# Optimization experiments

Hardware: AMD Instinct MI355X
Metric: run time of the kernel (lower is better)

Reference implementation:

```python
import jax, jax.numpy as jnp
import numpy as np

B, S, E, H = 2, 2048, 1024, 16
D = E // H
LN_EPS = 1e-5
NORM_EPS = 1e-12  # F.normalize clamp_min


def setup_inputs() -> dict:
    key = jax.random.key(0)
    ks = jax.random.split(key, 4)
    x = jax.random.normal(ks[0], (B, S, E), dtype=jnp.float32)
    qkv_w = jax.random.normal(ks[1], (3 * E, E), dtype=jnp.float32) * 0.02
    qkv_b = jnp.zeros((3 * E,), dtype=jnp.float32)
    out_w = jax.random.normal(ks[2], (E, E), dtype=jnp.float32) * 0.02
    out_b = jnp.zeros((E,), dtype=jnp.float32)
    ln_w = jnp.ones((E,), dtype=jnp.float32)
    ln_b = jnp.zeros((E,), dtype=jnp.float32)
    qknorm_scale = jnp.asarray(E ** -0.5, dtype=jnp.float32)
    # RotaryEmbedding buffer: inv_freq interleaved (emb[::2] = emb[1::2] = base**(-arange(0,E,2)/E))
    base_freq = 10000.0 ** (-(np.arange(0, E, 2).astype(np.float32) / E))
    emb = np.empty((E,), dtype=np.float32)
    emb[::2] = base_freq
    emb[1::2] = base_freq
    inv_freq = jnp.asarray(emb)
    return {"x": x, "ln_w": ln_w, "ln_b": ln_b, "qkv_w": qkv_w, "qkv_b": qkv_b,
            "qknorm_scale": qknorm_scale, "out_w": out_w, "out_b": out_b, "inv_freq": inv_freq}


def _rotate(t, sin, cos):
    # Faithful to source: x1 = even idx (excluding last), x2 = odd idx; cat(-x2, x1)
    x1 = t[..., :-1:2]
    x2 = t[..., 1::2]
    t_rot = jnp.concatenate((-x2, x1), axis=-1)
    return t * cos + t_rot * sin


def _l2norm(t):
    n = jnp.sqrt(jnp.sum(t * t, axis=-1, keepdims=True))
    return t / jnp.maximum(n, NORM_EPS)


def reference(x, ln_w, ln_b, qkv_w, qkv_b, qknorm_scale, out_w, out_b, inv_freq):
    # --- prenorm (LayerNorm, eps=1e-5) ---
    mu = jnp.mean(x, axis=-1, keepdims=True)
    var = jnp.mean((x - mu) ** 2, axis=-1, keepdims=True)
    xn = (x - mu) / jnp.sqrt(var + LN_EPS) * ln_w + ln_b
    # --- QKV projection ---
    qkv = xn @ qkv_w.T + qkv_b  # [B,S,3E]
    q, k, v = jnp.split(qkv, 3, axis=-1)
    # --- rotary (source uses scalar seq*inv_freq, not per-position) ---
    seq = q.shape[1]
    sin = jnp.sin(seq * inv_freq)
    cos = jnp.cos(seq * inv_freq)
    q = _rotate(q, sin, cos)
    k = _rotate(k, sin, cos)
    # --- split heads: [B,S,E] -> [B,H,S,D] ---
    split = lambda t: t.reshape(B, seq, H, D).transpose(0, 2, 1, 3)
    q, k, v = split(q), split(k), split(v)
    # --- qknorm ---
    q = _l2norm(q) * qknorm_scale
    k = _l2norm(k) * qknorm_scale
    # --- scaled dot product with causal mask ---
    aw = jnp.einsum('bhqd,bhkd->bhqk', q, k)  # [B,H,S,S]
    causal = jnp.tril(jnp.ones((seq, seq), dtype=bool))
    aw = jnp.where(causal, aw, jnp.finfo(aw.dtype).min)
    aw = jax.nn.softmax(aw, axis=-1)
    attn = jnp.einsum('bhqk,bhkd->bhqd', aw, v)
    # --- merge heads + out proj ---
    attn = attn.transpose(0, 2, 1, 3).reshape(B, seq, E)
    return attn @ out_w.T + out_b
```

## Files before the change

kernel.cpp:

```cpp
#include <hip/hip_runtime.h>

typedef unsigned short u16;
typedef __attribute__((ext_vector_type(8))) short bf16x8;
typedef __attribute__((ext_vector_type(4))) float f32x4;

#define SS 2048
#define EE 1024
#define HH 16
#define DD 64

__device__ __forceinline__ float b2f(u16 u) {
  union { unsigned int i; float f; } v; v.i = ((unsigned int)u) << 16; return v.f;
}
__device__ __forceinline__ u16 f2b(float f) {
  union { float f; unsigned int i; } v; v.f = f;
  unsigned int i = v.i;
  return (u16)((i + 0x7FFFu + ((i >> 16) & 1u)) >> 16);
}
__device__ __forceinline__ unsigned int cvt_pk_bf16(float lo, float hi) {
  unsigned int r;
  asm("v_cvt_pk_bf16_f32 %0, %1, %2" : "=v"(r) : "v"(lo), "v"(hi));
  return r;
}

#define GLD16(g, l)                                                         \
  __builtin_amdgcn_global_load_lds(                                         \
      (const __attribute__((address_space(1))) unsigned int*)(g),           \
      (__attribute__((address_space(3))) unsigned int*)(l), 16, 0, 0)

__global__ __launch_bounds__(256) void k_prep(const float* __restrict__ qkv_w,
                                              u16* __restrict__ wq_b,
                                              const float* __restrict__ inv_freq,
                                              float2* __restrict__ cs,
                                              const float* __restrict__ x,
                                              const float* __restrict__ lw,
                                              const float* __restrict__ lb,
                                              u16* __restrict__ xn) {
  const int bx = blockIdx.x, t = threadIdx.x;
  if (bx < 3072) {
    const int i = bx * 256 + t;
    float4 v = ((const float4*)qkv_w)[i];
    ushort4 o;
    o.x = f2b(v.x); o.y = f2b(v.y); o.z = f2b(v.z); o.w = f2b(v.w);
    ((ushort4*)wq_b)[i] = o;
    return;
  }
  if (bx < 3076) {
    const int i = (bx - 3072) * 256 + t;
    float th = 2048.0f * inv_freq[i];
    cs[i] = make_float2(cosf(th), sinf(th));
    return;
  }
  const int row = bx - 3076;
  float4 v = ((const float4*)(x + (size_t)row * EE))[t];
  float f0 = v.x, f1 = v.y, f2 = v.z, f3 = v.w;
  float s = f0 + f1 + f2 + f3;
  float ss = f0 * f0 + f1 * f1 + f2 * f2 + f3 * f3;
  for (int o = 1; o < 64; o <<= 1) { s += __shfl_xor(s, o); ss += __shfl_xor(ss, o); }
  __shared__ float red[8];
  int w = t >> 6;
  if ((t & 63) == 0) { red[w] = s; red[4 + w] = ss; }
  __syncthreads();
  s = red[0] + red[1] + red[2] + red[3];
  ss = red[4] + red[5] + red[6] + red[7];
  float mu = s * (1.0f / 1024.0f);
  float var = ss * (1.0f / 1024.0f) - mu * mu;
  float rstd = rsqrtf(var + 1e-5f);
  float4 wv = ((const float4*)lw)[t];
  float4 bv = ((const float4*)lb)[t];
  ushort4 o;
  o.x = f2b((f0 - mu) * rstd * wv.x + bv.x);
  o.y = f2b((f1 - mu) * rstd * wv.y + bv.y);
  o.z = f2b((f2 - mu) * rstd * wv.z + bv.z);
  o.w = f2b((f3 - mu) * rstd * wv.w + bv.w);
  ((ushort4*)(xn + (size_t)row * EE))[t] = o;
}

__global__ __launch_bounds__(256) void k_gemm_b(const u16* __restrict__ A,
                                                const u16* __restrict__ W,
                                                const float* __restrict__ bias,
                                                u16* __restrict__ C,
                                                int M, int N, int K) {
  __shared__ __align__(16) u16 As[128 * 32];
  __shared__ __align__(16) u16 Ws[128 * 32];
  const int t = threadIdx.x;
  const int m0 = blockIdx.y * 128, n0 = blockIdx.x * 128;
  const int lane = t & 63, w = t >> 6, quad = lane >> 4, l15 = lane & 15;
  const int wm = (w & 1) * 64, wn = (w >> 1) * 64;

  f32x4 zero4 = {0.f, 0.f, 0.f, 0.f};
  f32x4 acc[4][4];
  for (int mi = 0; mi < 4; mi++)
    for (int ni = 0; ni < 4; ni++) acc[mi][ni] = zero4;

  const u16* Ag = A + (size_t)(m0 + (t >> 2)) * K + (t & 3) * 8;
  const u16* Wg = W + (size_t)(n0 + (t >> 2)) * K + (t & 3) * 8;
  const size_t rowskip = (size_t)64 * K;

  for (int k0 = 0; k0 < K; k0 += 32) {
    GLD16(Ag + k0, As + t * 8);
    GLD16(Ag + rowskip + k0, As + 2048 + t * 8);
    GLD16(Wg + k0, Ws + t * 8);
    GLD16(Wg + rowskip + k0, Ws + 2048 + t * 8);
    __syncthreads();
    bf16x8 af[4], wf[4];
#pragma unroll
    for (int i = 0; i < 4; i++) {
      af[i] = *(const bf16x8*)(As + (wm + i * 16 + l15) * 32 + quad * 8);
      wf[i] = *(const bf16x8*)(Ws + (wn + i * 16 + l15) * 32 + quad * 8);
    }
#pragma unroll
    for (int mi = 0; mi < 4; mi++)
#pragma unroll
      for (int ni = 0; ni < 4; ni++)
        acc[mi][ni] = __builtin_amdgcn_mfma_f32_16x16x32_bf16(af[mi], wf[ni], acc[mi][ni], 0, 0, 0);
    __syncthreads();
  }
  for (int mi = 0; mi < 4; mi++)
    for (int ni = 0; ni < 4; ni++) {
      int col = n0 + wn + ni * 16 + l15;
      float bb = bias[col];
      for (int r = 0; r < 4; r++) {
        int grow = m0 + wm + mi * 16 + quad * 4 + r;
        C[(size_t)grow * N + col] = f2b(acc[mi][ni][r] + bb);
      }
    }
}

__global__ __launch_bounds__(256) void k_gemm_fw(const u16* __restrict__ A,
                                                 const float* __restrict__ W,
                                                 const float* __restrict__ bias,
                                                 float* __restrict__ C,
                                                 int M, int N, int K) {
  __shared__ __align__(16) u16 As[64 * 32];
  __shared__ __align__(16) u16 Ws[128 * 32];
  const int t = threadIdx.x;
  const int m0 = blockIdx.y * 64, n0 = blockIdx.x * 128;
  const int lane = t & 63, w = t >> 6, quad = lane >> 4, l15 = lane & 15;
  const int wm = (w & 1) * 32, wn = (w >> 1) * 64;

  f32x4 zero4 = {0.f, 0.f, 0.f, 0.f};
  f32x4 acc[2][4];
  for (int mi = 0; mi < 2; mi++)
    for (int ni = 0; ni < 4; ni++) acc[mi][ni] = zero4;

  const u16* Ag = A + (size_t)(m0 + (t >> 2)) * K + (t & 3) * 8;
  const float* Wg0 = W + (size_t)(n0 + (t >> 2)) * K + (t & 3) * 8;
  const float* Wg1 = Wg0 + (size_t)64 * K;

  for (int k0 = 0; k0 < K; k0 += 32) {
    GLD16(Ag + k0, As + t * 8);
    float4 wa = *(const float4*)(Wg0 + k0);
    float4 wb = *(const float4*)(Wg0 + k0 + 4);
    float4 wc = *(const float4*)(Wg1 + k0);
    float4 wd = *(const float4*)(Wg1 + k0 + 4);
    union { unsigned int u[4]; bf16x8 v8; } p0, p1;
    p0.u[0] = cvt_pk_bf16(wa.x, wa.y); p0.u[1] = cvt_pk_bf16(wa.z, wa.w);
    p0.u[2] = cvt_pk_bf16(wb.x, wb.y); p0.u[3] = cvt_pk_bf16(wb.z, wb.w);
    p1.u[0] = cvt_pk_bf16(wc.x, wc.y); p1.u[1] = cvt_pk_bf16(wc.z, wc.w);
    p1.u[2] = cvt_pk_bf16(wd.x, wd.y); p1.u[3] = cvt_pk_bf16(wd.z, wd.w);
    *(bf16x8*)(Ws + t * 8) = p0.v8;
    *(bf16x8*)(Ws + 2048 + t * 8) = p1.v8;
    __syncthreads();
    bf16x8 af[2], wf[4];
#pragma unroll
    for (int i = 0; i < 2; i++)
      af[i] = *(const bf16x8*)(As + (wm + i * 16 + l15) * 32 + quad * 8);
#pragma unroll
    for (int i = 0; i < 4; i++)
      wf[i] = *(const bf16x8*)(Ws + (wn + i * 16 + l15) * 32 + quad * 8);
#pragma unroll
    for (int mi = 0; mi < 2; mi++)
#pragma unroll
      for (int ni = 0; ni < 4; ni++)
        acc[mi][ni] = __builtin_amdgcn_mfma_f32_16x16x32_bf16(af[mi], wf[ni], acc[mi][ni], 0, 0, 0);
    __syncthreads();
  }
  for (int mi = 0; mi < 2; mi++)
    for (int ni = 0; ni < 4; ni++) {
      int col = n0 + wn + ni * 16 + l15;
      float bb = bias[col];
      for (int r = 0; r < 4; r++) {
        int grow = m0 + wm + mi * 16 + quad * 4 + r;
        C[(size_t)grow * N + col] = acc[mi][ni][r] + bb;
      }
    }
}

__global__ __launch_bounds__(256) void k_rotv(u16* __restrict__ qkv,
                                              const float2* __restrict__ cs_tab,
                                              const float* __restrict__ scale_p,
                                              u16* __restrict__ vt) {
  __shared__ float qf[1024];
  __shared__ float kf[1024];
  __shared__ __align__(16) u16 tile[64 * 72];
  const int row = blockIdx.x, t = threadIdx.x;
  {
    u16* qr = qkv + (size_t)row * 3072;
    u16* kr = qr + 1024;
    ushort4 qv = ((const ushort4*)qr)[t];
    ushort4 kv = ((const ushort4*)kr)[t];
    *(float4*)(qf + 4 * t) = make_float4(b2f(qv.x), b2f(qv.y), b2f(qv.z), b2f(qv.w));
    *(float4*)(kf + 4 * t) = make_float4(b2f(kv.x), b2f(kv.y), b2f(kv.z), b2f(kv.w));
    __syncthreads();
    const float scale = scale_p[0];
    float rq[4], rk[4];
#pragma unroll
    for (int u = 0; u < 4; u++) {
      int j = 4 * t + u;
      float2 cs = cs_tab[j];
      float qrot = (j < 512) ? -qf[2 * j + 1] : qf[2 * (j - 512)];
      float krot = (j < 512) ? -kf[2 * j + 1] : kf[2 * (j - 512)];
      rq[u] = qf[j] * cs.x + qrot * cs.y;
      rk[u] = kf[j] * cs.x + krot * cs.y;
    }
    float ssq = rq[0] * rq[0] + rq[1] * rq[1] + rq[2] * rq[2] + rq[3] * rq[3];
    float ssk = rk[0] * rk[0] + rk[1] * rk[1] + rk[2] * rk[2] + rk[3] * rk[3];
    for (int o = 1; o < 16; o <<= 1) { ssq += __shfl_xor(ssq, o); ssk += __shfl_xor(ssk, o); }
    float qs = scale / fmaxf(sqrtf(ssq), 1e-12f);
    float ks = scale / fmaxf(sqrtf(ssk), 1e-12f);
    ushort4 qo, ko;
    qo.x = f2b(rq[0] * qs); qo.y = f2b(rq[1] * qs); qo.z = f2b(rq[2] * qs); qo.w = f2b(rq[3] * qs);
    ko.x = f2b(rk[0] * ks); ko.y = f2b(rk[1] * ks); ko.z = f2b(rk[2] * ks); ko.w = f2b(rk[3] * ks);
    ((ushort4*)qr)[t] = qo;
    ((ushort4*)kr)[t] = ko;
  }
  if (row >= 1024) return;
  const int st = row & 31, bh = row >> 5;
  const int b = bh >> 4, h = bh & 15;
  const int s0 = st * 64;
  const int si = t >> 2, dc = t & 3;
  __syncthreads();
  const u16* src = qkv + (size_t)(b * SS + s0 + si) * 3072 + 2048 + h * DD;
  bf16x8 v0 = *(const bf16x8*)(src + dc * 8);
  bf16x8 v1 = *(const bf16x8*)(src + (dc + 4) * 8);
#pragma unroll
  for (int u = 0; u < 8; u++) tile[(dc * 8 + u) * 72 + si] = (u16)v0[u];
#pragma unroll
  for (int u = 0; u < 8; u++) tile[((dc + 4) * 8 + u) * 72 + si] = (u16)v1[u];
  __syncthreads();
#pragma unroll
  for (int it = 0; it < 2; it++) {
    int idx = t + it * 256;
    int d = idx >> 3, ch = idx & 7;
    bf16x8 o = *(const bf16x8*)(tile + d * 72 + ch * 8);
    *(bf16x8*)(vt + (size_t)(bh * DD + d) * SS + s0 + ch * 8) = o;
  }
}

__global__ __launch_bounds__(512, 4) void k_attn(const u16* __restrict__ qkv,
                                                 const u16* __restrict__ vt,
                                                 u16* __restrict__ out) {
  __shared__ __align__(16) u16 Kt[2][128 * 72];
  __shared__ __align__(16) u16 Vt[2][64 * 136];
  const int bh = blockIdx.x;
  const int y = blockIdx.y;
  const int qt = (y < 8) ? y : 23 - y;
  const int b = bh >> 4, h = bh & 15;
  const int t = threadIdx.x, w = t >> 6, lane = t & 63, quad = lane >> 4, l15 = lane & 15;
  const int krow = t >> 2, kq = (t & 3) * 16;
  const int dr = t >> 3, kc8 = t & 7;
  const int srcl = (lane & 48) + ((lane >> 4) << 2);
  const int qA = ((lane >> 4) & 1) * 32 + l15;
  const int qB = qA + 16;
  const bool hiN = (quad >> 1) & 1;
  const u16* kn = qkv + 1024;
  f32x4 zero4 = {0.f, 0.f, 0.f, 0.f};
  const int q0 = qt * 128;

  bf16x8 qf[2];
  {
    const u16* qrow = qkv + (size_t)(b * SS + q0 + 16 * w + l15) * 3072 + h * DD;
    qf[0] = *(const bf16x8*)(qrow + quad * 8);
    qf[1] = *(const bf16x8*)(qrow + 32 + quad * 8);
  }
  f32x4 oacc[4];
  for (int n = 0; n < 4; n++) oacc[n] = zero4;
  float m_i = -1e30f, l_i = 0.f;

  bf16x8 kv[2], vv[2];
  {
    const u16* krg = kn + (size_t)(b * SS + krow) * 3072 + h * DD + kq;
    kv[0] = *(const bf16x8*)(krg);
    kv[1] = *(const bf16x8*)(krg + 8);
    const u16* vrg = vt + (size_t)(bh * DD + dr) * SS + kc8 * 16;
    vv[0] = *(const bf16x8*)(vrg);
    vv[1] = *(const bf16x8*)(vrg + 8);
  }
  *(bf16x8*)(Kt[0] + krow * 72 + kq) = kv[0];
  *(bf16x8*)(Kt[0] + krow * 72 + kq + 8) = kv[1];
  *(bf16x8*)(Vt[0] + dr * 136 + kc8 * 16) = vv[0];
  *(bf16x8*)(Vt[0] + dr * 136 + kc8 * 16 + 8) = vv[1];
  __syncthreads();
  int cur = 0;

  for (int kt = 0; kt <= qt; kt++) {
    if (kt < qt) {
      const int k0n = (kt + 1) * 128;
      const u16* krg = kn + (size_t)(b * SS + k0n + krow) * 3072 + h * DD + kq;
      kv[0] = *(const bf16x8*)(krg);
      kv[1] = *(const bf16x8*)(krg + 8);
      const u16* vrg = vt + (size_t)(bh * DD + dr) * SS + k0n + kc8 * 16;
      vv[0] = *(const bf16x8*)(vrg);
      vv[1] = *(const bf16x8*)(vrg + 8);
    }
    const u16* Kc = Kt[cur];
    const u16* Vc = Vt[cur];
    f32x4 sacc[8];
#pragma unroll
    for (int n = 0; n < 8; n++) {
      sacc[n] = zero4;
#pragma unroll
      for (int c = 0; c < 2; c++) {
        bf16x8 kfrag = *(const bf16x8*)(Kc + (n * 16 + l15) * 72 + c * 32 + quad * 8);
        sacc[n] = __builtin_amdgcn_mfma_f32_16x16x32_bf16(kfrag, qf[c], sacc[n], 0, 0, 0);
      }
    }
    if (kt == qt) {
      const int qrow = 16 * w + l15, kbase = 4 * quad;
#pragma unroll
      for (int n = 0; n < 8; n++)
#pragma unroll
        for (int r = 0; r < 4; r++)
          if (16 * n + kbase + r > qrow) sacc[n][r] = -1e30f;
    }
    float mx = -1e30f;
#pragma unroll
    for (int n = 0; n < 8; n++)
#pragma unroll
      for (int r = 0; r < 4; r++) mx = fmaxf(mx, sacc[n][r]);
    mx = fmaxf(mx, __shfl_xor(mx, 16));
    mx = fmaxf(mx, __shfl_xor(mx, 32));
    float mn = fmaxf(m_i, mx);
    float al = __expf(m_i - mn);
    m_i = mn;
    float rs = 0.f;
#pragma unroll
    for (int n = 0; n < 8; n++)
#pragma unroll
      for (int r = 0; r < 4; r++) {
        float p = __expf(sacc[n][r] - mn);
        sacc[n][r] = p;
        rs += p;
      }
    rs += __shfl_xor(rs, 16);
    rs += __shfl_xor(rs, 32);
    l_i = al * l_i + rs;
    float alr[4];
#pragma unroll
    for (int r = 0; r < 4; r++) alr[r] = __shfl(al, srcl + r);
#pragma unroll
    for (int n = 0; n < 4; n++)
#pragma unroll
      for (int r = 0; r < 4; r++) oacc[n][r] *= alr[r];
    unsigned int pkw[8][2];
#pragma unroll
    for (int n = 0; n < 8; n++) {
      pkw[n][0] = cvt_pk_bf16(sacc[n][0], sacc[n][1]);
      pkw[n][1] = cvt_pk_bf16(sacc[n][2], sacc[n][3]);
    }
#pragma unroll
    for (int c = 0; c < 4; c++) {
      unsigned int a0 = __shfl(pkw[2 * c][0], qA);
      unsigned int a1 = __shfl(pkw[2 * c][1], qA);
      unsigned int a2 = __shfl(pkw[2 * c][0], qB);
      unsigned int a3 = __shfl(pkw[2 * c][1], qB);
      unsigned int b0 = __shfl(pkw[2 * c + 1][0], qA);
      unsigned int b1 = __shfl(pkw[2 * c + 1][1], qA);
      unsigned int b2 = __shfl(pkw[2 * c + 1][0], qB);
      unsigned int b3 = __shfl(pkw[2 * c + 1][1], qB);
      union { unsigned int u[4]; bf16x8 v8; } pf;
      pf.u[0] = hiN ? b0 : a0;
      pf.u[1] = hiN ? b1 : a1;
      pf.u[2] = hiN ? b2 : a2;
      pf.u[3] = hiN ? b3 : a3;
#pragma unroll
      for (int n = 0; n < 4; n++) {
        bf16x8 vf = *(const bf16x8*)(Vc + (n * 16 + l15) * 136 + c * 32 + quad * 8);
        oacc[n] = __builtin_amdgcn_mfma_f32_16x16x32_bf16(pf.v8, vf, oacc[n], 0, 0, 0);
      }
    }
    if (kt < qt) {
      *(bf16x8*)(Kt[cur ^ 1] + krow * 72 + kq) = kv[0];
      *(bf16x8*)(Kt[cur ^ 1] + krow * 72 + kq + 8) = kv[1];
      *(bf16x8*)(Vt[cur ^ 1] + dr * 136 + kc8 * 16) = vv[0];
      *(bf16x8*)(Vt[cur ^ 1] + dr * 136 + kc8 * 16 + 8) = vv[1];
    }
    __syncthreads();
    cur ^= 1;
  }
  float lr[4];
#pragma unroll
  for (int r = 0; r < 4; r++) lr[r] = __shfl(l_i, srcl + r);
  for (int n = 0; n < 4; n++)
    for (int r = 0; r < 4; r++) {
      int row = q0 + 16 * w + quad * 4 + r;
      out[(size_t)(b * SS + row) * EE + h * DD + n * 16 + l15] = f2b(oacc[n][r] / lr[r]);
    }
}

extern "C" void kernel_launch(void* const* d_in, const int* in_sizes, int n_in,
                              void* d_out, int out_size, void* d_ws, size_t ws_size,
                              hipStream_t stream) {
  const float* x       = (const float*)d_in[0];
  const float* ln_w    = (const float*)d_in[1];
  const float* ln_b    = (const float*)d_in[2];
  const float* qkv_w   = (const float*)d_in[3];
  const float* qkv_b   = (const float*)d_in[4];
  const float* qk_s    = (const float*)d_in[5];
  const float* out_w   = (const float*)d_in[6];
  const float* out_b   = (const float*)d_in[7];
  const float* inv_frq = (const float*)d_in[8];

  u16* ws   = (u16*)d_ws;
  u16* xn   = ws;
  u16* qkv  = ws + (size_t)4096 * 1024;
  u16* wq_b = (u16*)d_out;
  float2* cs_tab = (float2*)((char*)d_out + 6291456);
  u16* vt   = (u16*)d_out + (size_t)4194304;

  k_prep<<<7172, 256, 0, stream>>>(qkv_w, wq_b, inv_frq, cs_tab, x, ln_w, ln_b, xn);
  k_gemm_b<<<dim3(24, 32), 256, 0, stream>>>(xn, wq_b, qkv_b, qkv, 4096, 3072, 1024);
  k_rotv<<<4096, 256, 0, stream>>>(qkv, cs_tab, qk_s, vt);
  k_attn<<<dim3(32, 16), 512, 0, stream>>>(qkv, vt, xn);
  k_gemm_fw<<<dim3(8, 64), 256, 0, stream>>>(xn, out_w, out_b, (float*)d_out, 4096, 1024, 1024);
}
```

Measured before the change: 212.9 us.

## Fuse V transpose into QKV GEMM epilogue, add lazy softmax rescale and MFMA priority

The QKV GEMM epilogue now writes the V columns straight into the transposed [B,H,D,S] layout. This lets the rotary kernel drop its shared-memory V transpose pass and the extra read and write of V. The attention kernel skips the running-max update and the output rescale unless some lane's max grows by more than 8, which saves exp and multiply work per tile. It also raises wave priority around the MFMA blocks. The risks are scattered 8-byte stores in the GEMM epilogue and the lazy-rescale threshold, where exp of up to e^8 could reduce accuracy.

New measurement: 231.6 us. +8.8%, slower.

```diff
diff --git a/kernel.cpp b/kernel.cpp
--- a/kernel.cpp
+++ b/kernel.cpp
@@ -80,6 +80,7 @@
                                                 const u16* __restrict__ W,
                                                 const float* __restrict__ bias,
                                                 u16* __restrict__ C,
+                                                u16* __restrict__ VT,
                                                 int M, int N, int K) {
   __shared__ __align__(16) u16 As[128 * 32];
   __shared__ __align__(16) u16 Ws[128 * 32];
@@ -116,15 +117,33 @@
         acc[mi][ni] = __builtin_amdgcn_mfma_f32_16x16x32_bf16(af[mi], wf[ni], acc[mi][ni], 0, 0, 0);
     __syncthreads();
   }
-  for (int mi = 0; mi < 4; mi++)
-    for (int ni = 0; ni < 4; ni++) {
-      int col = n0 + wn + ni * 16 + l15;
-      float bb = bias[col];
-      for (int r = 0; r < 4; r++) {
-        int grow = m0 + wm + mi * 16 + quad * 4 + r;
-        C[(size_t)grow * N + col] = f2b(acc[mi][ni][r] + bb);
-      }
-    }
+  if (n0 < 2048) {
+    for (int mi = 0; mi < 4; mi++)
+      for (int ni = 0; ni < 4; ni++) {
+        int col = n0 + wn + ni * 16 + l15;
+        float bb = bias[col];
+        for (int r = 0; r < 4; r++) {
+          int grow = m0 + wm + mi * 16 + quad * 4 + r;
+          C[(size_t)grow * N + col] = f2b(acc[mi][ni][r] + bb);
+        }
+      }
+  } else {
+    for (int mi = 0; mi < 4; mi++)
+      for (int ni = 0; ni < 4; ni++) {
+        int col = n0 + wn + ni * 16 + l15;
+        int vcol = col - 2048;
+        int h = vcol >> 6, d = vcol & 63;
+        float bb = bias[col];
+        int grow0 = m0 + wm + mi * 16 + quad * 4;
+        int b = grow0 >> 11, s0 = grow0 & 2047;
+        ushort4 o;
+        o.x = f2b(acc[mi][ni][0] + bb);
+        o.y = f2b(acc[mi][ni][1] + bb);
+        o.z = f2b(acc[mi][ni][2] + bb);
+        o.w = f2b(acc[mi][ni][3] + bb);
+        *(ushort4*)(VT + ((size_t)((b * 16 + h) * 64 + d)) * SS + s0) = o;
+      }
+  }
 }
 
 __global__ __launch_bounds__(256) void k_gemm_fw(const u16* __restrict__ A,
@@ -189,63 +208,38 @@
 
 __global__ __launch_bounds__(256) void k_rotv(u16* __restrict__ qkv,
                                               const float2* __restrict__ cs_tab,
-                                              const float* __restrict__ scale_p,
-                                              u16* __restrict__ vt) {
+                                              const float* __restrict__ scale_p) {
   __shared__ float qf[1024];
   __shared__ float kf[1024];
-  __shared__ __align__(16) u16 tile[64 * 72];
   const int row = blockIdx.x, t = threadIdx.x;
-  {
-    u16* qr = qkv + (size_t)row * 3072;
-    u16* kr = qr + 1024;
-    ushort4 qv = ((const ushort4*)qr)[t];
-    ushort4 kv = ((const ushort4*)kr)[t];
-    *(float4*)(qf + 4 * t) = make_float4(b2f(qv.x), b2f(qv.y), b2f(qv.z), b2f(qv.w));
-    *(float4*)(kf + 4 * t) = make_float4(b2f(kv.x), b2f(kv.y), b2f(kv.z), b2f(kv.w));
-    __syncthreads();
-    const float scale = scale_p[0];
-    float rq[4], rk[4];
-#pragma unroll
-    for (int u = 0; u < 4; u++) {
-      int j = 4 * t + u;
-      float2 cs = cs_tab[j];
-      float qrot = (j < 512) ? -qf[2 * j + 1] : qf[2 * (j - 512)];
-      float krot = (j < 512) ? -kf[2 * j + 1] : kf[2 * (j - 512)];
-      rq[u] = qf[j] * cs.x + qrot * cs.y;
-      rk[u] = kf[j] * cs.x + krot * cs.y;
-    }
-    float ssq = rq[0] * rq[0] + rq[1] * rq[1] + rq[2] * rq[2] + rq[3] * rq[3];
-    float ssk = rk[0] * rk[0] + rk[1] * rk[1] + rk[2] * rk[2] + rk[3] * rk[3];
-    for (int o = 1; o < 16; o <<= 1) { ssq += __shfl_xor(ssq, o); ssk += __shfl_xor(ssk, o); }
-    float qs = scale / fmaxf(sqrtf(ssq), 1e-12f);
-    float ks = scale / fmaxf(sqrtf(ssk), 1e-12f);
-    ushort4 qo, ko;
-    qo.x = f2b(rq[0] * qs); qo.y = f2b(rq[1] * qs); qo.z = f2b(rq[2] * qs); qo.w = f2b(rq[3] * qs);
-    ko.x = f2b(rk[0] * ks); ko.y = f2b(rk[1] * ks); ko.z = f2b(rk[2] * ks); ko.w = f2b(rk[3] * ks);
-    ((ushort4*)qr)[t] = qo;
-    ((ushort4*)kr)[t] = ko;
-  }
-  if (row >= 1024) return;
-  const int st = row & 31, bh = row >> 5;
-  const int b = bh >> 4, h = bh & 15;
-  const int s0 = st * 64;
-  const int si = t >> 2, dc = t & 3;
+  u16* qr = qkv + (size_t)row * 3072;
+  u16* kr = qr + 1024;
+  ushort4 qv = ((const ushort4*)qr)[t];
+  ushort4 kv = ((const ushort4*)kr)[t];
+  *(float4*)(qf + 4 * t) = make_float4(b2f(qv.x), b2f(qv.y), b2f(qv.z), b2f(qv.w));
+  *(float4*)(kf + 4 * t) = make_float4(b2f(kv.x), b2f(kv.y), b2f(kv.z), b2f(kv.w));
   __syncthreads();
-  const u16* src = qkv + (size_t)(b * SS + s0 + si) * 3072 + 2048 + h * DD;
-  bf16x8 v0 = *(const bf16x8*)(src + dc * 8);
-  bf16x8 v1 = *(const bf16x8*)(src + (dc + 4) * 8);
-#pragma unroll
-  for (int u = 0; u < 8; u++) tile[(dc * 8 + u) * 72 + si] = (u16)v0[u];
-#pragma unroll
-  for (int u = 0; u < 8; u++) tile[((dc + 4) * 8 + u) * 72 + si] = (u16)v1[u];
-  __syncthreads();
-#pragma unroll
-  for (int it = 0; it < 2; it++) {
-    int idx = t + it * 256;
-    int d = idx >> 3, ch = idx & 7;
-    bf16x8 o = *(const bf16x8*)(tile + d * 72 + ch * 8);
-    *(bf16x8*)(vt + (size_t)(bh * DD + d) * SS + s0 + ch * 8) = o;
-  }
+  const float scale = scale_p[0];
+  float rq[4], rk[4];
+#pragma unroll
+  for (int u = 0; u < 4; u++) {
+    int j = 4 * t + u;
+    float2 cs = cs_tab[j];
+    float qrot = (j < 512) ? -qf[2 * j + 1] : qf[2 * (j - 512)];
+    float krot = (j < 512) ? -kf[2 * j + 1] : kf[2 * (j - 512)];
+    rq[u] = qf[j] * cs.x + qrot * cs.y;
+    rk[u] = kf[j] * cs.x + krot * cs.y;
+  }
+  float ssq = rq[0] * rq[0] + rq[1] * rq[1] + rq[2] * rq[2] + rq[3] * rq[3];
+  float ssk = rk[0] * rk[0] + rk[1] * rk[1] + rk[2] * rk[2] + rk[3] * rk[3];
+  for (int o = 1; o < 16; o <<= 1) { ssq += __shfl_xor(ssq, o); ssk += __shfl_xor(ssk, o); }
+  float qs = scale / fmaxf(sqrtf(ssq), 1e-12f);
+  float ks = scale / fmaxf(sqrtf(ssk), 1e-12f);
+  ushort4 qo, ko;
+  qo.x = f2b(rq[0] * qs); qo.y = f2b(rq[1] * qs); qo.z = f2b(rq[2] * qs); qo.w = f2b(rq[3] * qs);
+  ko.x = f2b(rk[0] * ks); ko.y = f2b(rk[1] * ks); ko.z = f2b(rk[2] * ks); ko.w = f2b(rk[3] * ks);
+  ((ushort4*)qr)[t] = qo;
+  ((ushort4*)kr)[t] = ko;
 }
 
 __global__ __launch_bounds__(512, 4) void k_attn(const u16* __restrict__ qkv,
@@ -307,6 +301,7 @@
     const u16* Kc = Kt[cur];
     const u16* Vc = Vt[cur];
     f32x4 sacc[8];
+    __builtin_amdgcn_s_setprio(1);
 #pragma unroll
     for (int n = 0; n < 8; n++) {
       sacc[n] = zero4;
@@ -316,6 +311,7 @@
         sacc[n] = __builtin_amdgcn_mfma_f32_16x16x32_bf16(kfrag, qf[c], sacc[n], 0, 0, 0);
       }
     }
+    __builtin_amdgcn_s_setprio(0);
     if (kt == qt) {
       const int qrow = 16 * w + l15, kbase = 4 * quad;
 #pragma unroll
@@ -331,28 +327,34 @@
       for (int r = 0; r < 4; r++) mx = fmaxf(mx, sacc[n][r]);
     mx = fmaxf(mx, __shfl_xor(mx, 16));
     mx = fmaxf(mx, __shfl_xor(mx, 32));
-    float mn = fmaxf(m_i, mx);
-    float al = __expf(m_i - mn);
-    m_i = mn;
+    const bool need = !__all(mx - m_i <= 8.0f);
+    float al = 1.0f;
+    if (need) {
+      float mn = fmaxf(m_i, mx);
+      al = __expf(m_i - mn);
+      m_i = mn;
+    }
     float rs = 0.f;
 #pragma unroll
     for (int n = 0; n < 8; n++)
 #pragma unroll
       for (int r = 0; r < 4; r++) {
-        float p = __expf(sacc[n][r] - mn);
+        float p = __expf(sacc[n][r] - m_i);
         sacc[n][r] = p;
         rs += p;
       }
     rs += __shfl_xor(rs, 16);
     rs += __shfl_xor(rs, 32);
     l_i = al * l_i + rs;
-    float alr[4];
-#pragma unroll
-    for (int r = 0; r < 4; r++) alr[r] = __shfl(al, srcl + r);
-#pragma unroll
-    for (int n = 0; n < 4; n++)
-#pragma unroll
-      for (int r = 0; r < 4; r++) oacc[n][r] *= alr[r];
+    if (need) {
+      float alr[4];
+#pragma unroll
+      for (int r = 0; r < 4; r++) alr[r] = __shfl(al, srcl + r);
+#pragma unroll
+      for (int n = 0; n < 4; n++)
+#pragma unroll
+        for (int r = 0; r < 4; r++) oacc[n][r] *= alr[r];
+    }
     unsigned int pkw[8][2];
 #pragma unroll
     for (int n = 0; n < 8; n++) {
@@ -374,11 +376,13 @@
       pf.u[1] = hiN ? b1 : a1;
       pf.u[2] = hiN ? b2 : a2;
       pf.u[3] = hiN ? b3 : a3;
+      __builtin_amdgcn_s_setprio(1);
 #pragma unroll
       for (int n = 0; n < 4; n++) {
         bf16x8 vf = *(const bf16x8*)(Vc + (n * 16 + l15) * 136 + c * 32 + quad * 8);
         oacc[n] = __builtin_amdgcn_mfma_f32_16x16x32_bf16(pf.v8, vf, oacc[n], 0, 0, 0);
       }
+      __builtin_amdgcn_s_setprio(0);
     }
     if (kt < qt) {
       *(bf16x8*)(Kt[cur ^ 1] + krow * 72 + kq) = kv[0];
@@ -420,8 +424,8 @@
   u16* vt   = (u16*)d_out + (size_t)4194304;
 
   k_prep<<<7172, 256, 0, stream>>>(qkv_w, wq_b, inv_frq, cs_tab, x, ln_w, ln_b, xn);
-  k_gemm_b<<<dim3(24, 32), 256, 0, stream>>>(xn, wq_b, qkv_b, qkv, 4096, 3072, 1024);
-  k_rotv<<<4096, 256, 0, stream>>>(qkv, cs_tab, qk_s, vt);
+  k_gemm_b<<<dim3(24, 32), 256, 0, stream>>>(xn, wq_b, qkv_b, qkv, vt, 4096, 3072, 1024);
+  k_rotv<<<4096, 256, 0, stream>>>(qkv, cs_tab, qk_s);
   k_attn<<<dim3(32, 16), 512, 0, stream>>>(qkv, vt, xn);
   k_gemm_fw<<<dim3(8, 64), 256, 0, stream>>>(xn, out_w, out_b, (float*)d_out, 4096, 1024, 1024);
 }
```
